# Optimization experiments

Measured on AMD Instinct MI355X. Metric: run time of the kernel, lower is better.

Reference implementation:

```python
import jax, jax.numpy as jnp
import numpy as np

N_GRAPH = 100000
N_CAND = 10
N_TOTAL = N_GRAPH + N_CAND
F_IN = 128
N_TYPES = 10
E = 6400000


def _p(key, shape, scale=0.05):
    return scale * jax.random.normal(key, shape, dtype=jnp.float32)


def setup_inputs() -> dict:
    key = jax.random.key(0)
    ks = jax.random.split(key, 20)
    x = jax.random.normal(ks[0], (N_GRAPH, F_IN), dtype=jnp.float32)
    candidate_set = jax.random.normal(ks[1], (N_CAND, F_IN), dtype=jnp.float32)
    edge_index = jax.random.randint(ks[2], (2, E), 0, N_GRAPH, dtype=jnp.int64)
    candidate_idx = jnp.arange(N_GRAPH, N_TOTAL, dtype=jnp.int64)  # candidate nodes appended last
    return {
        "x": x, "candidate_set": candidate_set,
        "edge_index": edge_index, "candidate_idx": candidate_idx,
        "W1": _p(ks[3], (F_IN, 16)), "b1": jnp.zeros((16,), jnp.float32),
        "W2": _p(ks[4], (16, 24)), "b2": jnp.zeros((24,), jnp.float32),
        "W3": _p(ks[5], (24, 32)), "b3": jnp.zeros((32,), jnp.float32),
        "Ws1": _p(ks[6], (32, 16)), "bs1": jnp.zeros((16,), jnp.float32),
        "Ws2": _p(ks[7], (16, N_TYPES)), "bs2": jnp.zeros((N_TYPES,), jnp.float32),
        "We1": _p(ks[8], (32, 24)), "be1": jnp.zeros((24,), jnp.float32),
        "We2": _p(ks[9], (24, N_TYPES)), "be2": jnp.zeros((N_TYPES,), jnp.float32),
    }


def _gcn(h, src, dst, W, b, n):
    # GCNConv: x' = D^{-1/2}(A+I)D^{-1/2} X W + b (self-loops added)
    h = h @ W
    deg = jax.ops.segment_sum(jnp.ones(src.shape, h.dtype), dst, num_segments=n) + 1.0
    dinv = jax.lax.rsqrt(deg)
    msg = h[src] * (dinv[src] * dinv[dst])[:, None]
    out = jax.ops.segment_sum(msg, dst, num_segments=n)
    out = out + h * (dinv * dinv)[:, None]  # self-loop term
    return out + b


def relu6(x):
    return jnp.clip(x, 0.0, 6.0)


def reference(x, candidate_set, edge_index, candidate_idx,
              W1, b1, W2, b2, W3, b3,
              Ws1, bs1, Ws2, bs2, We1, be1, We2, be2):
    n = N_TOTAL
    src, dst = edge_index[0], edge_index[1]
    h = jnp.concatenate([x, candidate_set], axis=0)  # [n, F_IN]
    h = _gcn(h, src, dst, W1, b1, n)
    h = _gcn(h, src, dst, W2, b2, n)
    h = _gcn(h, src, dst, W3, b3, n)  # [n, 32]

    start_probs = jax.nn.softmax(relu6(h @ Ws1 + bs1) @ Ws2 + bs2, axis=0)  # [n, T]
    mask = jnp.ones_like(start_probs).at[candidate_idx].set(0.0)
    start_probs = start_probs * mask
    start_probs = jnp.where(start_probs == 0.0, 1e-10, start_probs)
    k1, k2 = jax.random.split(jax.random.key(42))
    start_node = jax.random.categorical(k1, jnp.log(start_probs), axis=-1)  # [n]

    combined = jnp.concatenate([h, h[start_node]], axis=0)  # [2n, 32]
    end_probs = jax.nn.softmax(relu6(combined @ We1 + be1) @ We2 + be2, axis=0)  # [2n, T]
    end_probs = end_probs.at[start_node].set(0.0)
    end_probs = jnp.where(end_probs == 0.0, 1e-10, end_probs)
    end_node = jax.random.categorical(k2, jnp.log(end_probs), axis=-1)  # [2n]
    return (start_node, end_node, start_probs, end_probs)
```

## Files before the change

kernel.cpp:

```cpp
#include <hip/hip_runtime.h>
#include <stdint.h>

constexpr int N_GRAPH = 100000;
constexpr int N_CANDS = 10;
constexpr int NT      = N_GRAPH + N_CANDS;
constexpr int F_IN    = 128;
constexpr int NTYPES  = 10;
constexpr int NE      = 6400000;

constexpr int CB_SHIFT = 9;
constexpr int CB       = 1 << CB_SHIFT;
constexpr int NBK2     = (NT + CB - 1) / CB;
constexpr int SB       = 512;
constexpr int NMAT     = NBK2 * SB;
constexpr int NSCAN_B  = NMAT / 256;
constexpr int TMPENT_CAP = NE + NMAT * 15 + 16;

#define RNG_VARIANT 0

__device__ __forceinline__ void tf2x32(uint32_t k0, uint32_t k1, uint32_t x0, uint32_t x1,
                                       uint32_t& o0, uint32_t& o1) {
  const uint32_t ks2 = k0 ^ k1 ^ 0x1BD11BDAu;
  uint32_t v0 = x0 + k0, v1 = x1 + k1;
#define TFR(r) { v0 += v1; v1 = (v1 << (r)) | (v1 >> (32 - (r))); v1 ^= v0; }
  TFR(13) TFR(15) TFR(26) TFR(6)
  v0 += k1;  v1 += ks2 + 1u;
  TFR(17) TFR(29) TFR(16) TFR(24)
  v0 += ks2; v1 += k0 + 2u;
  TFR(13) TFR(15) TFR(26) TFR(6)
  v0 += k0;  v1 += k1 + 3u;
  TFR(17) TFR(29) TFR(16) TFR(24)
  v0 += k1;  v1 += ks2 + 4u;
  TFR(13) TFR(15) TFR(26) TFR(6)
  v0 += ks2; v1 += k0 + 5u;
#undef TFR
  o0 = v0; o1 = v1;
}

__device__ __forceinline__ void derive_keys(uint32_t& a0, uint32_t& a1,
                                            uint32_t& b0, uint32_t& b1) {
#if RNG_VARIANT == 2
  uint32_t c0, c1, d0, d1;
  tf2x32(0u, 42u, 0u, 2u, c0, c1);
  tf2x32(0u, 42u, 1u, 3u, d0, d1);
  a0 = c0; a1 = d0; b0 = c1; b1 = d1;
#else
  tf2x32(0u, 42u, 0u, 0u, a0, a1);
  tf2x32(0u, 42u, 0u, 1u, b0, b1);
#endif
}

__device__ __forceinline__ uint32_t rng_bits(uint32_t k0, uint32_t k1,
                                             uint32_t idx, uint32_t total) {
#if RNG_VARIANT == 0
  uint32_t o0, o1; tf2x32(k0, k1, 0u, idx, o0, o1); return o0 ^ o1;
#elif RNG_VARIANT == 1
  uint32_t o0, o1; tf2x32(k0, k1, 0u, idx, o0, o1); return o1;
#else
  uint32_t half = total >> 1; uint32_t o0, o1;
  if (idx < half) { tf2x32(k0, k1, idx, idx + half, o0, o1); return o0; }
  tf2x32(k0, k1, idx - half, idx, o0, o1); return o1;
#endif
}

__device__ __forceinline__ double gumbel_from_bits(uint32_t bits) {
  float uf = __uint_as_float((bits >> 9) | 0x3f800000u) - 1.0f;
  uf = fmaxf(1.17549435e-38f, uf + 1.17549435e-38f);
  return -log(-log((double)uf));
}

__device__ __forceinline__ uint32_t encf(float f) {
  uint32_t u = __float_as_uint(f);
  return u ^ ((u & 0x80000000u) ? 0xFFFFFFFFu : 0x80000000u);
}
__device__ __forceinline__ float decf(uint32_t e) {
  uint32_t u = (e & 0x80000000u) ? (e ^ 0x80000000u) : ~e;
  return __uint_as_float(u);
}

__global__ __launch_bounds__(512) void k_bcount(const int* __restrict__ dst,
                                                int* __restrict__ cntmat,
                                                int* __restrict__ cnt) {
  __shared__ int h[NBK2];
  int tid = threadIdx.x, blk = blockIdx.x;
  for (int b = tid; b < NBK2; b += 512) h[b] = 0;
  __syncthreads();
  int per = (NE + SB - 1) / SB;
  int e0 = blk * per, e1 = min(e0 + per, NE);
  for (int e = e0 + tid; e < e1; e += 512) atomicAdd(&h[dst[e] >> CB_SHIFT], 1);
  __syncthreads();
  for (int b = tid; b < NBK2; b += 512) {
    int c = h[b];
    cntmat[b * SB + blk] = (c + 15) & ~15;
    if (c) atomicAdd(&cnt[b], c);
  }
}

__global__ __launch_bounds__(256) void k_s1(int* __restrict__ cmat, int* __restrict__ partial) {
  __shared__ int sm[256];
  int t = blockIdx.x * 256 + threadIdx.x;
  int v = cmat[t];
  sm[threadIdx.x] = v;
  __syncthreads();
  #pragma unroll
  for (int s = 1; s < 256; s <<= 1) {
    int a = (threadIdx.x >= s) ? sm[threadIdx.x - s] : 0;
    __syncthreads();
    sm[threadIdx.x] += a;
    __syncthreads();
  }
  cmat[t] = sm[threadIdx.x] - v;
  if (threadIdx.x == 255) partial[blockIdx.x] = sm[255];
}

__global__ __launch_bounds__(512) void k_s2(int* __restrict__ partial, int* __restrict__ cmat) {
  __shared__ int sm[512];
  int t = threadIdx.x;
  int v = (t < NSCAN_B) ? partial[t] : 0;
  sm[t] = v;
  __syncthreads();
  #pragma unroll
  for (int s = 1; s < 512; s <<= 1) {
    int a = (t >= s) ? sm[t - s] : 0;
    __syncthreads();
    sm[t] += a;
    __syncthreads();
  }
  if (t < NSCAN_B) partial[t] = sm[t] - v;
  if (t == 511) cmat[NMAT] = sm[511];
}

__global__ __launch_bounds__(256) void k_s3(int* __restrict__ cmat, const int* __restrict__ partial) {
  int t = blockIdx.x * 256 + threadIdx.x;
  cmat[t] += partial[blockIdx.x];
}

__global__ __launch_bounds__(256) void k_rowscan(const int* __restrict__ cnt,
                                                 int* __restrict__ rowbase) {
  __shared__ int sm[256];
  int t = threadIdx.x;
  int v = (t < NBK2) ? cnt[t] : 0;
  sm[t] = v;
  __syncthreads();
  #pragma unroll
  for (int s = 1; s < 256; s <<= 1) {
    int a = (t >= s) ? sm[t - s] : 0;
    __syncthreads();
    sm[t] += a;
    __syncthreads();
  }
  if (t < NBK2) rowbase[t] = sm[t] - v;
}

__global__ __launch_bounds__(512) void k_scatter2(const int* __restrict__ src,
                                                  const int* __restrict__ dst,
                                                  const int* __restrict__ cmat,
                                                  uint32_t* __restrict__ tmpent) {
  __shared__ int lcur[NBK2];
  int tid = threadIdx.x, blk = blockIdx.x;
  for (int b = tid; b < NBK2; b += 512) lcur[b] = cmat[b * SB + blk];
  __syncthreads();
  int per = (NE + SB - 1) / SB;
  int e0 = blk * per, e1 = min(e0 + per, NE);
  for (int e = e0 + tid; e < e1; e += 512) {
    int s = src[e], d = dst[e];
    int b = d >> CB_SHIFT;
    int pos = atomicAdd(&lcur[b], 1);
    tmpent[pos] = (uint32_t)s | ((uint32_t)(d & (CB - 1)) << 17);
  }
  __syncthreads();
  for (int b = tid; b < NBK2; b += 512) {
    int p = lcur[b];
    int end = cmat[b * SB + blk + 1];
    for (; p < end; ++p) tmpent[p] = 0xFFFFFFFFu;
  }
}

__global__ __launch_bounds__(512) void k_place(const uint32_t* __restrict__ tmpent,
                                               const int* __restrict__ cmat,
                                               const int* __restrict__ rowbase,
                                               int* __restrict__ rowptr,
                                               float* __restrict__ dinv,
                                               int* __restrict__ col) {
  __shared__ int sdeg[CB];
  __shared__ int sexc[CB];
  __shared__ int sscan[CB];
  int b = blockIdx.x, tid = threadIdx.x;
  sdeg[tid] = 0;
  __syncthreads();
  int r0 = cmat[b * SB], r1 = cmat[(b + 1) * SB];
  for (int e = r0 + tid; e < r1; e += 512) {
    uint32_t v = tmpent[e];
    if (v != 0xFFFFFFFFu) atomicAdd(&sdeg[v >> 17], 1);
  }
  __syncthreads();
  int d = sdeg[tid];
  sscan[tid] = d;
  __syncthreads();
  #pragma unroll
  for (int s = 1; s < CB; s <<= 1) {
    int v = (tid >= s) ? sscan[tid - s] : 0;
    __syncthreads();
    sscan[tid] += v;
    __syncthreads();
  }
  int rb = rowbase[b];
  int incl = rb + sscan[tid];
  sexc[tid] = incl - d;
  int i = b * CB + tid;
  if (i < NT) {
    rowptr[i + 1] = incl;
    dinv[i] = (float)(1.0 / sqrt((double)(d + 1)));
  }
  if (b == 0 && tid == 0) rowptr[0] = 0;
  __syncthreads();
  for (int e = r0 + tid; e < r1; e += 512) {
    uint32_t v = tmpent[e];
    if (v != 0xFFFFFFFFu) {
      int pos = atomicAdd(&sexc[v >> 17], 1);
      col[pos] = (int)(v & 0x1FFFFu);
    }
  }
}

__global__ __launch_bounds__(256) void k_mm1(const float* __restrict__ x, const float* __restrict__ cand,
                                             const float* __restrict__ W, const float* __restrict__ dinv,
                                             float* __restrict__ g) {
  int gid = blockIdx.x * 256 + threadIdx.x;
  if (gid >= NT * 16) return;
  int i = gid >> 4, f = gid & 15;
  const float* hr = (i < N_GRAPH) ? (x + (size_t)i * F_IN)
                                  : (cand + (size_t)(i - N_GRAPH) * F_IN);
  double a = 0.0;
  #pragma unroll 8
  for (int k = 0; k < F_IN; ++k) a += (double)hr[k] * (double)W[k * 16 + f];
  g[gid] = (float)(a * (double)dinv[i]);
}

template <int FI, int FO>
__global__ __launch_bounds__(256) void k_mm(const float* __restrict__ H, const float* __restrict__ W,
                                            const float* __restrict__ dinv, float* __restrict__ g) {
  int gid = blockIdx.x * 256 + threadIdx.x;
  if (gid >= NT * FO) return;
  int i = gid / FO, f = gid - i * FO;
  const float* hr = H + (size_t)i * FI;
  double a = 0.0;
  #pragma unroll
  for (int k = 0; k < FI; ++k) a += (double)hr[k] * (double)W[k * FO + f];
  g[gid] = (float)(a * (double)dinv[i]);
}

template <int F, int R>
__global__ __launch_bounds__(F * R) void k_gcn(const int* __restrict__ rowptr,
                                               const int* __restrict__ col,
                                               const float* __restrict__ g,
                                               const float* __restrict__ dinv,
                                               const float* __restrict__ b,
                                               float* __restrict__ Hn) {
  int i = blockIdx.x * R + threadIdx.y;
  if (i >= NT) return;
  int f = threadIdx.x;
  int e0 = rowptr[i], e1 = rowptr[i + 1];
  double acc = 0.0;
  int e = e0;
  for (; e + 4 <= e1; e += 4) {
    int c0 = col[e], c1 = col[e + 1], c2 = col[e + 2], c3 = col[e + 3];
    float v0 = g[(size_t)c0 * F + f];
    float v1 = g[(size_t)c1 * F + f];
    float v2 = g[(size_t)c2 * F + f];
    float v3 = g[(size_t)c3 * F + f];
    acc += (double)v0 + (double)v1 + (double)v2 + (double)v3;
  }
  for (; e < e1; ++e) acc += (double)g[(size_t)col[e] * F + f];
  acc += (double)g[(size_t)i * F + f];
  Hn[(size_t)i * F + f] = (float)((double)dinv[i] * acc + (double)b[f]);
}

template <int HID>
__global__ __launch_bounds__(256) void k_head(const float* __restrict__ H, const int* __restrict__ sn,
                                              int nrows,
                                              const float* __restrict__ Wa, const float* __restrict__ ba,
                                              const float* __restrict__ Wb, const float* __restrict__ bb,
                                              float* __restrict__ logits) {
  int i = blockIdx.x * 256 + threadIdx.x;
  if (i >= nrows) return;
  int row = (i < NT) ? i : sn[i - NT];
  const float* hr = H + (size_t)row * 32;
  float h[32];
  #pragma unroll
  for (int k = 0; k < 32; ++k) h[k] = hr[k];
  double hid[HID];
  for (int j = 0; j < HID; ++j) {
    double a = (double)ba[j];
    #pragma unroll
    for (int k = 0; k < 32; ++k) a += (double)h[k] * (double)Wa[k * HID + j];
    hid[j] = fmin(fmax(a, 0.0), 6.0);
  }
  for (int t = 0; t < NTYPES; ++t) {
    double l = (double)bb[t];
    #pragma unroll
    for (int j = 0; j < HID; ++j) l += hid[j] * (double)Wb[j * NTYPES + t];
    logits[(size_t)i * NTYPES + t] = (float)l;
  }
}

__global__ __launch_bounds__(256) void k_colmax(const float* __restrict__ L, int nrows,
                                                uint32_t* __restrict__ mb) {
  __shared__ float sm[256][NTYPES];
  float m[NTYPES];
  #pragma unroll
  for (int t = 0; t < NTYPES; ++t) m[t] = -3.402823466e38f;
  for (int r = blockIdx.x * 256 + threadIdx.x; r < nrows; r += gridDim.x * 256) {
    #pragma unroll
    for (int t = 0; t < NTYPES; ++t) m[t] = fmaxf(m[t], L[(size_t)r * NTYPES + t]);
  }
  #pragma unroll
  for (int t = 0; t < NTYPES; ++t) sm[threadIdx.x][t] = m[t];
  __syncthreads();
  for (int s = 128; s > 0; s >>= 1) {
    if (threadIdx.x < s)
      for (int t = 0; t < NTYPES; ++t)
        sm[threadIdx.x][t] = fmaxf(sm[threadIdx.x][t], sm[threadIdx.x + s][t]);
    __syncthreads();
  }
  if (threadIdx.x < NTYPES) atomicMax(&mb[threadIdx.x], encf(sm[0][threadIdx.x]));
}

__global__ __launch_bounds__(256) void k_colsum(const float* __restrict__ L, int nrows,
                                                const uint32_t* __restrict__ mb,
                                                double* __restrict__ sums) {
  __shared__ double sm[256][NTYPES];
  float mx[NTYPES];
  #pragma unroll
  for (int t = 0; t < NTYPES; ++t) mx[t] = decf(mb[t]);
  double s[NTYPES];
  #pragma unroll
  for (int t = 0; t < NTYPES; ++t) s[t] = 0.0;
  for (int r = blockIdx.x * 256 + threadIdx.x; r < nrows; r += gridDim.x * 256) {
    #pragma unroll
    for (int t = 0; t < NTYPES; ++t)
      s[t] += exp((double)L[(size_t)r * NTYPES + t] - (double)mx[t]);
  }
  #pragma unroll
  for (int t = 0; t < NTYPES; ++t) sm[threadIdx.x][t] = s[t];
  __syncthreads();
  for (int st = 128; st > 0; st >>= 1) {
    if (threadIdx.x < st)
      for (int t = 0; t < NTYPES; ++t)
        sm[threadIdx.x][t] += sm[threadIdx.x + st][t];
    __syncthreads();
  }
  if (threadIdx.x < NTYPES) atomicAdd(&sums[threadIdx.x], sm[0][threadIdx.x]);
}

__global__ __launch_bounds__(256) void k_probs_start(const float* __restrict__ L,
                                                     const uint32_t* __restrict__ mb,
                                                     const double* __restrict__ sums,
                                                     float* __restrict__ P) {
  int gid = blockIdx.x * 256 + threadIdx.x;
  if (gid >= NT * NTYPES) return;
  int i = gid / NTYPES, t = gid - i * NTYPES;
  double p = exp((double)L[gid] - (double)decf(mb[t])) / sums[t];
  float pf = (float)p;
  if (i >= N_GRAPH || pf == 0.0f) pf = 1e-10f;
  P[gid] = pf;
}

__global__ __launch_bounds__(256) void k_probs_end(const float* __restrict__ L,
                                                   const uint32_t* __restrict__ mb,
                                                   const double* __restrict__ sums,
                                                   const int* __restrict__ flags,
                                                   float* __restrict__ P) {
  int gid = blockIdx.x * 256 + threadIdx.x;
  if (gid >= 2 * NT * NTYPES) return;
  int j = gid / NTYPES, t = gid - j * NTYPES;
  double p = exp((double)L[gid] - (double)decf(mb[t])) / sums[t];
  float pf = (float)p;
  if ((j < NTYPES && flags[j]) || pf == 0.0f) pf = 1e-10f;
  P[gid] = pf;
}

__global__ __launch_bounds__(256) void k_sample_start(const float* __restrict__ probs,
                                                      float* __restrict__ outSN,
                                                      int* __restrict__ sn, int* __restrict__ flags) {
  int i = blockIdx.x * 256 + threadIdx.x;
  if (i >= NT) return;
  uint32_t a0, a1, b0, b1; derive_keys(a0, a1, b0, b1);
  double best = -1e300; int bi = 0;
  #pragma unroll
  for (int t = 0; t < NTYPES; ++t) {
    uint32_t bits = rng_bits(a0, a1, (uint32_t)(i * NTYPES + t), (uint32_t)(NT * NTYPES));
    double v = log((double)probs[(size_t)i * NTYPES + t]) + gumbel_from_bits(bits);
    if (v > best) { best = v; bi = t; }
  }
  sn[i] = bi;
  outSN[i] = (float)bi;
  flags[bi] = 1;
}

__global__ __launch_bounds__(256) void k_sample_end(const float* __restrict__ probs,
                                                    float* __restrict__ outEN) {
  int j = blockIdx.x * 256 + threadIdx.x;
  if (j >= 2 * NT) return;
  uint32_t a0, a1, b0, b1; derive_keys(a0, a1, b0, b1);
  double best = -1e300; int bi = 0;
  #pragma unroll
  for (int t = 0; t < NTYPES; ++t) {
    uint32_t bits = rng_bits(b0, b1, (uint32_t)(j * NTYPES + t), (uint32_t)(2 * NT * NTYPES));
    double v = log((double)probs[(size_t)j * NTYPES + t]) + gumbel_from_bits(bits);
    if (v > best) { best = v; bi = t; }
  }
  outEN[j] = (float)bi;
}

extern "C" void kernel_launch(void* const* d_in, const int* in_sizes, int n_in,
                              void* d_out, int out_size, void* d_ws, size_t ws_size,
                              hipStream_t stream) {
  const float* x    = (const float*)d_in[0];
  const float* cand = (const float*)d_in[1];
  const int*   ei   = (const int*)d_in[2];
  const float* W1 = (const float*)d_in[4];  const float* b1 = (const float*)d_in[5];
  const float* W2 = (const float*)d_in[6];  const float* b2 = (const float*)d_in[7];
  const float* W3 = (const float*)d_in[8];  const float* b3 = (const float*)d_in[9];
  const float* Ws1 = (const float*)d_in[10]; const float* bs1 = (const float*)d_in[11];
  const float* Ws2 = (const float*)d_in[12]; const float* bs2 = (const float*)d_in[13];
  const float* We1 = (const float*)d_in[14]; const float* be1 = (const float*)d_in[15];
  const float* We2 = (const float*)d_in[16]; const float* be2 = (const float*)d_in[17];
  float* out = (float*)d_out;
  float* outSN = out;
  float* outEN = out + NT;
  float* outPS = out + 3 * NT;
  float* outPE = out + 13 * NT;

  char* ws = (char*)d_ws;
  size_t off = 0;
  auto alloc = [&](size_t bytes) -> void* {
    void* p = ws + off;
    off += (bytes + 511) & ~(size_t)511;
    return p;
  };
  float*    dinv    = (float*)alloc((size_t)NT * 4);
  float*    g       = (float*)alloc((size_t)NT * 32 * 4);
  float*    Ha      = (float*)alloc((size_t)NT * 32 * 4);
  int*      rowptr  = (int*)alloc((size_t)(NT + 1) * 4);
  int*      cnt     = (int*)alloc((size_t)NBK2 * 4);
  int*      rowbase = (int*)alloc((size_t)NBK2 * 4);
  int*      cmat    = (int*)alloc((size_t)(NMAT + 1) * 4);
  int*      partial = (int*)alloc(512 * 4);
  int*      col     = (int*)alloc((size_t)NE * 4);
  char*     ublk    = (char*)alloc((size_t)TMPENT_CAP * 4);
  uint32_t* tmpent  = (uint32_t*)ublk;
  float*    Hb      = (float*)ublk;
  float*    logitsS = (float*)(ublk + (size_t)NT * 32 * 4);
  float*    logitsE = (float*)(ublk + (size_t)NT * 32 * 4 + (size_t)NT * NTYPES * 4);
  int*      sn      = (int*)alloc((size_t)NT * 4);
  uint32_t* maxS    = (uint32_t*)alloc(64);
  double*   sumS    = (double*)alloc(128);
  uint32_t* maxE    = (uint32_t*)alloc(64);
  double*   sumE    = (double*)alloc(128);
  int*      flags   = (int*)alloc(64);
  (void)ws_size; (void)in_sizes; (void)n_in; (void)out_size;

  const int* srcA = ei;
  const int* dstA = ei + NE;

  const int B = 256;
  auto blocks = [](long long nthreads) { return (int)((nthreads + 255) / 256); };

  hipMemsetAsync(cnt, 0, (size_t)NBK2 * 4, stream);
  k_bcount<<<SB, 512, 0, stream>>>(dstA, cmat, cnt);
  k_s1<<<NSCAN_B, 256, 0, stream>>>(cmat, partial);
  k_s2<<<1, 512, 0, stream>>>(partial, cmat);
  k_s3<<<NSCAN_B, 256, 0, stream>>>(cmat, partial);
  k_rowscan<<<1, 256, 0, stream>>>(cnt, rowbase);
  k_scatter2<<<SB, 512, 0, stream>>>(srcA, dstA, cmat, tmpent);
  k_place<<<NBK2, 512, 0, stream>>>(tmpent, cmat, rowbase, rowptr, dinv, col);

  k_mm1<<<blocks((long long)NT * 16), B, 0, stream>>>(x, cand, W1, dinv, g);
  k_gcn<16, 16><<<(NT + 15) / 16, dim3(16, 16), 0, stream>>>(rowptr, col, g, dinv, b1, Ha);

  k_mm<16, 24><<<blocks((long long)NT * 24), B, 0, stream>>>(Ha, W2, dinv, g);
  k_gcn<24, 10><<<(NT + 9) / 10, dim3(24, 10), 0, stream>>>(rowptr, col, g, dinv, b2, Hb);

  k_mm<24, 32><<<blocks((long long)NT * 32), B, 0, stream>>>(Hb, W3, dinv, g);
  k_gcn<32, 8><<<(NT + 7) / 8, dim3(32, 8), 0, stream>>>(rowptr, col, g, dinv, b3, Ha);

  k_head<16><<<blocks(NT), B, 0, stream>>>(Ha, sn, NT, Ws1, bs1, Ws2, bs2, logitsS);
  hipMemsetAsync(maxS, 0, (size_t)((char*)flags - (char*)maxS) + 512, stream);
  k_colmax<<<512, B, 0, stream>>>(logitsS, NT, maxS);
  k_colsum<<<512, B, 0, stream>>>(logitsS, NT, maxS, sumS);
  k_probs_start<<<blocks((long long)NT * NTYPES), B, 0, stream>>>(logitsS, maxS, sumS, outPS);
  k_sample_start<<<blocks(NT), B, 0, stream>>>(outPS, outSN, sn, flags);

  k_head<24><<<blocks(2 * NT), B, 0, stream>>>(Ha, sn, 2 * NT, We1, be1, We2, be2, logitsE);
  k_colmax<<<512, B, 0, stream>>>(logitsE, 2 * NT, maxE);
  k_colsum<<<512, B, 0, stream>>>(logitsE, 2 * NT, maxE, sumE);
  k_probs_end<<<blocks((long long)2 * NT * NTYPES), B, 0, stream>>>(logitsE, maxE, sumE, flags, outPE);
  k_sample_end<<<blocks(2 * NT), B, 0, stream>>>(outPE, outEN);
}
```

Measured before the change: 825.5 us.

## Fold GCN layer weights algebraically to propagate 16-wide features through all three layers

Because the GCN layers have no nonlinearity between them, the three propagations are reassociated so that each one moves a 16-wide feature matrix (X·W1) instead of 16/24/32-wide ones. The bias contributions are carried by separate scalar propagations (w1, w2), and the combined W2·W3 matrix plus the bias vectors are built in a small precomputed kernel. An epilogue then reconstructs the 32-wide layer-3 output. This is meant to cut gather traffic in the two wider propagations and uses float4 loads, at the cost of extra scalar gathers and floating-point rounding that differs from the reference.

```diff
diff --git a/kernel.cpp b/kernel.cpp
--- a/kernel.cpp
+++ b/kernel.cpp
@@ -225,55 +225,129 @@
 
 __global__ __launch_bounds__(256) void k_mm1(const float* __restrict__ x, const float* __restrict__ cand,
                                              const float* __restrict__ W, const float* __restrict__ dinv,
-                                             float* __restrict__ g) {
+                                             float* __restrict__ zs0) {
   int gid = blockIdx.x * 256 + threadIdx.x;
-  if (gid >= NT * 16) return;
-  int i = gid >> 4, f = gid & 15;
+  if (gid >= NT * 4) return;
+  int i = gid >> 2, f4 = gid & 3;
   const float* hr = (i < N_GRAPH) ? (x + (size_t)i * F_IN)
                                   : (cand + (size_t)(i - N_GRAPH) * F_IN);
-  double a = 0.0;
+  const float4* h4 = reinterpret_cast<const float4*>(hr);
+  const float4* W4 = reinterpret_cast<const float4*>(W);
+  double a0 = 0.0, a1 = 0.0, a2 = 0.0, a3 = 0.0;
   #pragma unroll 8
-  for (int k = 0; k < F_IN; ++k) a += (double)hr[k] * (double)W[k * 16 + f];
-  g[gid] = (float)(a * (double)dinv[i]);
-}
-
-template <int FI, int FO>
-__global__ __launch_bounds__(256) void k_mm(const float* __restrict__ H, const float* __restrict__ W,
-                                            const float* __restrict__ dinv, float* __restrict__ g) {
-  int gid = blockIdx.x * 256 + threadIdx.x;
-  if (gid >= NT * FO) return;
-  int i = gid / FO, f = gid - i * FO;
-  const float* hr = H + (size_t)i * FI;
-  double a = 0.0;
-  #pragma unroll
-  for (int k = 0; k < FI; ++k) a += (double)hr[k] * (double)W[k * FO + f];
-  g[gid] = (float)(a * (double)dinv[i]);
-}
-
-template <int F, int R>
-__global__ __launch_bounds__(F * R) void k_gcn(const int* __restrict__ rowptr,
-                                               const int* __restrict__ col,
-                                               const float* __restrict__ g,
-                                               const float* __restrict__ dinv,
-                                               const float* __restrict__ b,
-                                               float* __restrict__ Hn) {
+  for (int q = 0; q < 32; ++q) {
+    float4 hv = h4[q];
+    float4 w0 = W4[(4 * q + 0) * 4 + f4];
+    float4 w1 = W4[(4 * q + 1) * 4 + f4];
+    float4 w2 = W4[(4 * q + 2) * 4 + f4];
+    float4 w3 = W4[(4 * q + 3) * 4 + f4];
+    a0 += (double)hv.x * w0.x + (double)hv.y * w1.x + (double)hv.z * w2.x + (double)hv.w * w3.x;
+    a1 += (double)hv.x * w0.y + (double)hv.y * w1.y + (double)hv.z * w2.y + (double)hv.w * w3.y;
+    a2 += (double)hv.x * w0.z + (double)hv.y * w1.z + (double)hv.z * w2.z + (double)hv.w * w3.z;
+    a3 += (double)hv.x * w0.w + (double)hv.y * w1.w + (double)hv.z * w2.w + (double)hv.w * w3.w;
+  }
+  double di = (double)dinv[i];
+  float4 o;
+  o.x = (float)(a0 * di); o.y = (float)(a1 * di);
+  o.z = (float)(a2 * di); o.w = (float)(a3 * di);
+  reinterpret_cast<float4*>(zs0)[(size_t)i * 4 + f4] = o;
+}
+
+template <bool SQ, bool WITHW, int R>
+__global__ __launch_bounds__(4 * R) void k_prop(const int* __restrict__ rowptr,
+                                                const int* __restrict__ col,
+                                                const float* __restrict__ zin,
+                                                const float* __restrict__ win,
+                                                const float* __restrict__ dinv,
+                                                float* __restrict__ zout,
+                                                float* __restrict__ wout,
+                                                float* __restrict__ wsout) {
   int i = blockIdx.x * R + threadIdx.y;
   if (i >= NT) return;
-  int f = threadIdx.x;
+  int fx = threadIdx.x;
+  const float4* z4 = reinterpret_cast<const float4*>(zin);
   int e0 = rowptr[i], e1 = rowptr[i + 1];
-  double acc = 0.0;
+  double a0 = 0.0, a1 = 0.0, a2 = 0.0, a3 = 0.0, wa = 0.0;
   int e = e0;
   for (; e + 4 <= e1; e += 4) {
     int c0 = col[e], c1 = col[e + 1], c2 = col[e + 2], c3 = col[e + 3];
-    float v0 = g[(size_t)c0 * F + f];
-    float v1 = g[(size_t)c1 * F + f];
-    float v2 = g[(size_t)c2 * F + f];
-    float v3 = g[(size_t)c3 * F + f];
-    acc += (double)v0 + (double)v1 + (double)v2 + (double)v3;
-  }
-  for (; e < e1; ++e) acc += (double)g[(size_t)col[e] * F + f];
-  acc += (double)g[(size_t)i * F + f];
-  Hn[(size_t)i * F + f] = (float)((double)dinv[i] * acc + (double)b[f]);
+    float4 v0 = z4[(size_t)c0 * 4 + fx];
+    float4 v1 = z4[(size_t)c1 * 4 + fx];
+    float4 v2 = z4[(size_t)c2 * 4 + fx];
+    float4 v3 = z4[(size_t)c3 * 4 + fx];
+    if (WITHW && fx == 0)
+      wa += (double)win[c0] + (double)win[c1] + (double)win[c2] + (double)win[c3];
+    a0 += (double)v0.x + (double)v1.x + (double)v2.x + (double)v3.x;
+    a1 += (double)v0.y + (double)v1.y + (double)v2.y + (double)v3.y;
+    a2 += (double)v0.z + (double)v1.z + (double)v2.z + (double)v3.z;
+    a3 += (double)v0.w + (double)v1.w + (double)v2.w + (double)v3.w;
+  }
+  for (; e < e1; ++e) {
+    int c = col[e];
+    float4 v = z4[(size_t)c * 4 + fx];
+    if (WITHW && fx == 0) wa += (double)win[c];
+    a0 += (double)v.x; a1 += (double)v.y; a2 += (double)v.z; a3 += (double)v.w;
+  }
+  float4 s = z4[(size_t)i * 4 + fx];
+  a0 += (double)s.x; a1 += (double)s.y; a2 += (double)s.z; a3 += (double)s.w;
+  double di = (double)dinv[i];
+  double sc = SQ ? di * di : di;
+  float4 o;
+  o.x = (float)(sc * a0); o.y = (float)(sc * a1);
+  o.z = (float)(sc * a2); o.w = (float)(sc * a3);
+  reinterpret_cast<float4*>(zout)[(size_t)i * 4 + fx] = o;
+  if (WITHW && fx == 0) {
+    wa += (double)win[i];
+    double w = di * wa;
+    wout[i]  = (float)w;
+    wsout[i] = (float)(di * w);
+  }
+}
+
+__global__ __launch_bounds__(512) void k_small(const float* __restrict__ W2, const float* __restrict__ b2p,
+                                               const float* __restrict__ W3, const float* __restrict__ b1p,
+                                               double* __restrict__ M, double* __restrict__ u,
+                                               double* __restrict__ v) {
+  __shared__ double t[24];
+  int tid = threadIdx.x;
+  if (tid < 24) {
+    double a = 0.0;
+    for (int k = 0; k < 16; ++k) a += (double)b1p[k] * (double)W2[k * 24 + tid];
+    t[tid] = a;
+  }
+  if (tid >= 32 && tid < 64) {
+    int o = tid - 32;
+    double a = 0.0;
+    for (int j = 0; j < 24; ++j) a += (double)b2p[j] * (double)W3[j * 32 + o];
+    v[o] = a;
+  }
+  __syncthreads();
+  if (tid < 32) {
+    double a = 0.0;
+    for (int j = 0; j < 24; ++j) a += t[j] * (double)W3[j * 32 + tid];
+    u[tid] = a;
+  }
+  {
+    int k = tid >> 5, o = tid & 31;
+    double a = 0.0;
+    for (int j = 0; j < 24; ++j) a += (double)W2[k * 24 + j] * (double)W3[j * 32 + o];
+    M[tid] = a;
+  }
+}
+
+__global__ __launch_bounds__(256) void k_epi(const float* __restrict__ z3, const float* __restrict__ w1,
+                                             const float* __restrict__ w2,
+                                             const double* __restrict__ M, const double* __restrict__ u,
+                                             const double* __restrict__ v, const float* __restrict__ b3,
+                                             float* __restrict__ H) {
+  int gid = blockIdx.x * 256 + threadIdx.x;
+  if (gid >= NT * 32) return;
+  int i = gid >> 5, o = gid & 31;
+  const float* zr = z3 + (size_t)i * 16;
+  double acc = (double)b3[o] + (double)w2[i] * u[o] + (double)w1[i] * v[o];
+  #pragma unroll
+  for (int k = 0; k < 16; ++k) acc += (double)zr[k] * M[k * 32 + o];
+  H[gid] = (float)acc;
 }
 
 template <int HID>
@@ -440,8 +514,6 @@
     return p;
   };
   float*    dinv    = (float*)alloc((size_t)NT * 4);
-  float*    g       = (float*)alloc((size_t)NT * 32 * 4);
-  float*    Ha      = (float*)alloc((size_t)NT * 32 * 4);
   int*      rowptr  = (int*)alloc((size_t)(NT + 1) * 4);
   int*      cnt     = (int*)alloc((size_t)NBK2 * 4);
   int*      rowbase = (int*)alloc((size_t)NBK2 * 4);
@@ -450,9 +522,18 @@
   int*      col     = (int*)alloc((size_t)NE * 4);
   char*     ublk    = (char*)alloc((size_t)TMPENT_CAP * 4);
   uint32_t* tmpent  = (uint32_t*)ublk;
-  float*    Hb      = (float*)ublk;
-  float*    logitsS = (float*)(ublk + (size_t)NT * 32 * 4);
-  float*    logitsE = (float*)(ublk + (size_t)NT * 32 * 4 + (size_t)NT * NTYPES * 4);
+  float*    zsA     = (float*)ublk;
+  float*    zsB     = (float*)(ublk + (size_t)NT * 16 * 4);
+  float*    Ha      = (float*)(ublk + (size_t)NT * 16 * 4 * 2);
+  float*    logitsS = (float*)alloc((size_t)NT * NTYPES * 4);
+  float*    logitsE = (float*)alloc((size_t)2 * NT * NTYPES * 4);
+  float*    w1v     = (float*)alloc((size_t)NT * 4);
+  float*    ws1v    = (float*)alloc((size_t)NT * 4);
+  float*    w2v     = (float*)alloc((size_t)NT * 4);
+  float*    wsd     = (float*)alloc((size_t)NT * 4);
+  double*   Md      = (double*)alloc(512 * 8);
+  double*   ud      = (double*)alloc(32 * 8);
+  double*   vd      = (double*)alloc(32 * 8);
   int*      sn      = (int*)alloc((size_t)NT * 4);
   uint32_t* maxS    = (uint32_t*)alloc(64);
   double*   sumS    = (double*)alloc(128);
@@ -476,14 +557,13 @@
   k_scatter2<<<SB, 512, 0, stream>>>(srcA, dstA, cmat, tmpent);
   k_place<<<NBK2, 512, 0, stream>>>(tmpent, cmat, rowbase, rowptr, dinv, col);
 
-  k_mm1<<<blocks((long long)NT * 16), B, 0, stream>>>(x, cand, W1, dinv, g);
-  k_gcn<16, 16><<<(NT + 15) / 16, dim3(16, 16), 0, stream>>>(rowptr, col, g, dinv, b1, Ha);
-
-  k_mm<16, 24><<<blocks((long long)NT * 24), B, 0, stream>>>(Ha, W2, dinv, g);
-  k_gcn<24, 10><<<(NT + 9) / 10, dim3(24, 10), 0, stream>>>(rowptr, col, g, dinv, b2, Hb);
-
-  k_mm<24, 32><<<blocks((long long)NT * 32), B, 0, stream>>>(Hb, W3, dinv, g);
-  k_gcn<32, 8><<<(NT + 7) / 8, dim3(32, 8), 0, stream>>>(rowptr, col, g, dinv, b3, Ha);
+  k_small<<<1, 512, 0, stream>>>(W2, b2, W3, b1, Md, ud, vd);
+  k_mm1<<<blocks((long long)NT * 4), B, 0, stream>>>(x, cand, W1, dinv, zsA);
+  const int PR = 64, PBLK = (NT + PR - 1) / PR;
+  k_prop<true,  true,  PR><<<PBLK, dim3(4, PR), 0, stream>>>(rowptr, col, zsA, dinv, dinv, zsB, w1v, ws1v);
+  k_prop<true,  true,  PR><<<PBLK, dim3(4, PR), 0, stream>>>(rowptr, col, zsB, ws1v, dinv, zsA, w2v, wsd);
+  k_prop<false, false, PR><<<PBLK, dim3(4, PR), 0, stream>>>(rowptr, col, zsA, nullptr, dinv, zsB, nullptr, nullptr);
+  k_epi<<<blocks((long long)NT * 32), B, 0, stream>>>(zsB, w1v, w2v, Md, ud, vd, b3, Ha);
 
   k_head<16><<<blocks(NT), B, 0, stream>>>(Ha, sn, NT, Ws1, bs1, Ws2, bs2, logitsS);
   hipMemsetAsync(maxS, 0, (size_t)((char*)flags - (char*)maxS) + 512, stream);
```

Result: faster. 791.9 us (-4.1%).
